# Kernel optimization log

Measured on AMD Instinct MI355X. Metric: run time of the kernel, lower is better.

Reference implementation:

```python
import jax, jax.numpy as jnp
import numpy as np

B, S, H = 2, 2048, 1024
NH, HD = 16, 64  # num_heads, head_size


def setup_inputs() -> dict:
    key = jax.random.key(0)
    ks = jax.random.split(key, 8)
    return {
        "x": jax.random.normal(ks[0], (B, S, H), dtype=jnp.float32),
        "attn_mask": jax.random.randint(ks[1], (B, S, S), 0, 2, dtype=jnp.int32),
        "Wq": jax.random.normal(ks[2], (H, H), dtype=jnp.float32) * 0.02,
        "bq": jax.random.normal(ks[3], (H,), dtype=jnp.float32) * 0.02,
        "Wk": jax.random.normal(ks[4], (H, H), dtype=jnp.float32) * 0.02,
        "bk": jax.random.normal(ks[5], (H,), dtype=jnp.float32) * 0.02,
        "Wv": jax.random.normal(ks[6], (H, H), dtype=jnp.float32) * 0.02,
        "bv": jax.random.normal(ks[7], (H,), dtype=jnp.float32) * 0.02,
    }


def reference(x, attn_mask, Wq, bq, Wk, bk, Wv, bv):
    b, s, h = x.shape
    # QKV projections (self-attention: kv = attention_input)
    q = (jnp.einsum('bih,hx->bix', x, Wq) + bq).reshape(b, s, NH, HD)
    k = (jnp.einsum('bih,hx->bix', x, Wk) + bk).reshape(b, s, NH, HD)
    v = (jnp.einsum('bih,hx->bix', x, Wv) + bv).reshape(b, s, NH, HD)
    scale = 1.0 / (HD ** 0.5)
    # [B, NH, Sq, Skv] score matrix, additive mask, softmax
    attn_score = jnp.einsum('bind,bjnd->bnij', q, k) * scale
    adder = attn_mask.astype(jnp.float32)[:, None, :, :] * -10000.0
    attn_prob = jax.nn.softmax(attn_score + adder, axis=-1)
    # dropout is identity (training=False)
    attn_vec = jnp.einsum('bnij,bjnd->bind', attn_prob, v)
    return attn_vec.reshape(b, s, NH * HD)
```

## Files before the change

### kernel.cpp

```cpp
#include <hip/hip_runtime.h>
#include <hip/hip_bf16.h>
#include <math.h>


#define DI __device__ __forceinline__

typedef unsigned short u16;
typedef unsigned int u32;
typedef unsigned long long u64;
typedef __attribute__((ext_vector_type(8))) short bf16x8;
typedef __attribute__((ext_vector_type(4))) float f32x4;

constexpr int BB = 2, SS = 2048, HH = 1024, NHEAD = 16, HDIM = 64;

DI u16 f2bf(float f) {
  __hip_bfloat16 h = __float2bfloat16(f);
  union { __hip_bfloat16 h; u16 u; } c; c.h = h; return c.u;
}

DI void gload_lds16(const void* g, const void* l) {
  __builtin_amdgcn_global_load_lds(
      (const __attribute__((address_space(1))) u32*)(u64)g,
      (__attribute__((address_space(3))) u32*)(u32)(u64)l,
      16, 0, 0);
}

__global__ void xcast(const float* __restrict__ x, u16* __restrict__ xb) {
  const size_t i = ((size_t)blockIdx.x * 256 + threadIdx.x) * 8;
  float4 f0 = *(const float4*)(x + i);
  float4 f1 = *(const float4*)(x + i + 4);
  bf16x8 v;
  v[0] = (short)f2bf(f0.x); v[1] = (short)f2bf(f0.y);
  v[2] = (short)f2bf(f0.z); v[3] = (short)f2bf(f0.w);
  v[4] = (short)f2bf(f1.x); v[5] = (short)f2bf(f1.y);
  v[6] = (short)f2bf(f1.z); v[7] = (short)f2bf(f1.w);
  *(bf16x8*)(xb + i) = v;
}

__global__ void wtrans(const float* __restrict__ Wq, const float* __restrict__ Wk,
                       const float* __restrict__ Wv, u16* __restrict__ WT) {
  __shared__ u16 tile[64][65];
  const float* W = (blockIdx.z == 0) ? Wq : (blockIdx.z == 1) ? Wk : Wv;
  u16* Wt = WT + (size_t)blockIdx.z * HH * HH;
  const int n0 = blockIdx.x * 64, k0 = blockIdx.y * 64;
  for (int i = threadIdx.x; i < 64 * 64; i += 256) {
    int r = i >> 6, c = i & 63;
    tile[r][c] = f2bf(W[(size_t)(k0 + r) * HH + n0 + c]);
  }
  __syncthreads();
  for (int i = threadIdx.x; i < 64 * 64; i += 256) {
    int r = i >> 6, c = i & 63;
    Wt[(size_t)(n0 + r) * HH + k0 + c] = tile[c][r];
  }
}

__global__ void maskpack(const int* __restrict__ mask, u64* __restrict__ mb) {
  const size_t idx = (size_t)blockIdx.x * 256 + threadIdx.x;
  const int v = mask[idx];
  const u64 bal = __ballot(v != 0);
  if ((threadIdx.x & 63) == 0) mb[idx >> 6] = bal;
}

__global__ __launch_bounds__(256) void qkv_gemm(
    const u16* __restrict__ X, const u16* __restrict__ WTall,
    const float* __restrict__ bq, const float* __restrict__ bk,
    const float* __restrict__ bv,
    u16* __restrict__ Qo, u16* __restrict__ Ko, u16* __restrict__ Vo) {
  __shared__ alignas(128) u16 As[128 * 64];
  __shared__ alignas(128) u16 Bs[128 * 64];

  const int z = blockIdx.z;
  const u16* Wt = WTall + (size_t)z * HH * HH;
  const float* bias = (z == 0) ? bq : (z == 1) ? bk : bv;
  u16* Out = (z == 0) ? Qo : (z == 1) ? Ko : Vo;
  const float oscale = (z == 0) ? 0.18033688011112042f : 1.0f;

  const int tid = threadIdx.x;
  const int lane = tid & 63;
  const int w = tid >> 6;
  const int wm = (w >> 1) * 64, wn = (w & 1) * 64;
  const int lr = lane & 15, lkg = lane >> 4;
  const int m0 = blockIdx.y * 128, n0 = blockIdx.x * 128;

  u32 srow[4], scol[4];
#pragma unroll
  for (int i = 0; i < 4; ++i) {
    u32 f = i * 4096 + w * 1024 + lane * 16;
    u32 g = f ^ (((f >> 7) & 7) << 4);
    srow[i] = g >> 7;
    scol[i] = (g & 127) >> 1;
  }

  u32 aoff[4][2], boff[4][2];
#pragma unroll
  for (int mf = 0; mf < 4; ++mf)
#pragma unroll
    for (int ks = 0; ks < 2; ++ks) {
      int row = wm + mf * 16 + lr;
      aoff[mf][ks] = (u32)((row * 128 + ks * 64 + lkg * 16) ^ ((row & 7) << 4));
      row = wn + mf * 16 + lr;
      boff[mf][ks] = (u32)((row * 128 + ks * 64 + lkg * 16) ^ ((row & 7) << 4));
    }

  f32x4 acc[4][4];
#pragma unroll
  for (int i = 0; i < 4; ++i)
#pragma unroll
    for (int j = 0; j < 4; ++j) acc[i][j] = {0.f, 0.f, 0.f, 0.f};

  const u16* Xb = X + (size_t)m0 * HH;
  const u16* Wb = Wt + (size_t)n0 * HH;

  auto stage = [&](int kt) {
    const int k0 = kt * 64;
#pragma unroll
    for (int i = 0; i < 4; ++i) {
      gload_lds16(Xb + (size_t)srow[i] * HH + k0 + scol[i],
                  (const char*)As + i * 4096 + w * 1024);
      gload_lds16(Wb + (size_t)srow[i] * HH + k0 + scol[i],
                  (const char*)Bs + i * 4096 + w * 1024);
    }
  };

  stage(0);
  const int NT = HH / 64;
  for (int kt = 0; kt < NT; ++kt) {
    __syncthreads();
    bf16x8 a[2][4], bfr[2][4];
#pragma unroll
    for (int ks = 0; ks < 2; ++ks)
#pragma unroll
      for (int i = 0; i < 4; ++i) {
        a[ks][i] = *(const bf16x8*)((const char*)As + aoff[i][ks]);
        bfr[ks][i] = *(const bf16x8*)((const char*)Bs + boff[i][ks]);
      }
    __syncthreads();
    if (kt + 1 < NT) stage(kt + 1);
    __builtin_amdgcn_s_setprio(1);
#pragma unroll
    for (int ks = 0; ks < 2; ++ks)
#pragma unroll
      for (int mf = 0; mf < 4; ++mf)
#pragma unroll
        for (int nf = 0; nf < 4; ++nf)
          acc[mf][nf] = __builtin_amdgcn_mfma_f32_16x16x32_bf16(
              a[ks][mf], bfr[ks][nf], acc[mf][nf], 0, 0, 0);
    __builtin_amdgcn_s_setprio(0);
  }

#pragma unroll
  for (int mf = 0; mf < 4; ++mf)
#pragma unroll
    for (int nf = 0; nf < 4; ++nf) {
      const int gn = n0 + wn + nf * 16 + lr;
      const float bvv = bias[gn];
      const int nh = gn >> 6, hd = gn & 63;
#pragma unroll
      for (int r = 0; r < 4; ++r) {
        const int gm = m0 + wm + mf * 16 + lkg * 4 + r;
        const int bb = gm >> 11, ss = gm & 2047;
        const float v = (acc[mf][nf][r] + bvv) * oscale;
        if (z < 2)
          Out[(((size_t)bb * NHEAD + nh) * SS + ss) * HDIM + hd] = f2bf(v);
        else
          Out[(((size_t)bb * NHEAD + nh) * HDIM + hd) * SS + ss] = f2bf(v);
      }
    }
}

__global__ __launch_bounds__(512) void attn(
    const u16* __restrict__ Q, const u16* __restrict__ K,
    const u16* __restrict__ Vt, const u64* __restrict__ mb,
    float* __restrict__ out) {
  __shared__ alignas(128) char smem[16384 + 16384 + 8 * 16 * 72 * 2];
  u16* Ks = (u16*)smem;
  u16* Vs = (u16*)(smem + 16384);
  typedef u16 PsRow[16][72];
  PsRow* Ps = (PsRow*)(smem + 32768);
  float* cmb = (float*)smem;

  const int nh = blockIdx.x, qt = blockIdx.y, b = blockIdx.z;
  const int bnh = b * NHEAD + nh;
  const u16* Qh = Q + (size_t)bnh * SS * HDIM;
  const u16* Kh = K + (size_t)bnh * SS * HDIM;
  const u16* Vh = Vt + (size_t)bnh * HDIM * SS;
  const int q0 = qt * 64;

  const int tid = threadIdx.x, lane = tid & 63, w = tid >> 6;
  const int g = w >> 2, wg = w & 3;
  const int lr = lane & 15, lkg = lane >> 4;
  const int qrow_lane = q0 + wg * 16 + lr;
  const int kvbase = g * (SS / 2);

  bf16x8 qf[2];
#pragma unroll
  for (int h = 0; h < 2; ++h)
    qf[h] = *(const bf16x8*)(Qh + (size_t)qrow_lane * HDIM + h * 32 + lkg * 8);

  u32 srow[2], scol[2];
#pragma unroll
  for (int i = 0; i < 2; ++i) {
    u32 f = i * 4096 + wg * 1024 + lane * 16;
    u32 gg = f ^ (((f >> 7) & 7) << 4);
    srow[i] = gg >> 7;
    scol[i] = (gg & 127) >> 1;
  }

  auto stage = [&](int t) {
    const int kv0 = kvbase + t * 64;
#pragma unroll
    for (int i = 0; i < 2; ++i) {
      gload_lds16(Kh + (size_t)(kv0 + srow[i]) * HDIM + scol[i],
                  (const char*)(Ks + g * 4096) + i * 4096 + wg * 1024);
      gload_lds16(Vh + (size_t)srow[i] * SS + kv0 + scol[i],
                  (const char*)(Vs + g * 4096) + i * 4096 + wg * 1024);
    }
  };

  u32 koff[4][2];
#pragma unroll
  for (int i = 0; i < 4; ++i)
#pragma unroll
    for (int h = 0; h < 2; ++h) {
      int row = i * 16 + lr;
      koff[i][h] = (u32)((row * 128 + h * 64 + lkg * 16) ^ ((row & 7) << 4));
    }

  bf16x8 ones;
#pragma unroll
  for (int j = 0; j < 8; ++j) ones[j] = (short)0x3F80;

  f32x4 oacc[4];
  f32x4 lacc = {0.f, 0.f, 0.f, 0.f};
#pragma unroll
  for (int n = 0; n < 4; ++n) oacc[n] = {0.f, 0.f, 0.f, 0.f};

  stage(0);
  const int NT = SS / 128;
  const char* Kbase = (const char*)(Ks + g * 4096);
  const char* Vbase = (const char*)(Vs + g * 4096);
  for (int t = 0; t < NT; ++t) {
    __syncthreads();

    const u64 sh =
        mb[((size_t)b * SS + qrow_lane) * (SS / 64) + g * NT + t] >> (lkg * 4);
    const u32 w01 = (u32)sh, w23 = (u32)(sh >> 32);

    f32x4 sacc[4];
#pragma unroll
    for (int kvb = 0; kvb < 4; ++kvb) sacc[kvb] = {0.f, 0.f, 0.f, 0.f};
    __builtin_amdgcn_s_setprio(1);
#pragma unroll
    for (int kvb = 0; kvb < 4; ++kvb)
#pragma unroll
      for (int h = 0; h < 2; ++h) {
        const bf16x8 kf = *(const bf16x8*)(Kbase + koff[kvb][h]);
        sacc[kvb] = __builtin_amdgcn_mfma_f32_16x16x32_bf16(
            kf, qf[h], sacc[kvb], 0, 0, 0);
      }
    __builtin_amdgcn_s_setprio(0);

#pragma unroll
    for (int kvb = 0; kvb < 4; ++kvb) {
      const u32 word = (kvb < 2) ? w01 : w23;
      const int sb = (kvb & 1) * 16;
      union { u16 h[4]; u64 d; } pk;
#pragma unroll
      for (int r = 0; r < 4; ++r) {
        float s = sacc[kvb][r];
        s = ((word >> (sb + r)) & 1u) ? -14000.0f : s;
        pk.h[r] = f2bf(__builtin_amdgcn_exp2f(s));
      }
      *(u64*)&Ps[w][lr][kvb * 16 + lkg * 4] = pk.d;
    }

    __builtin_amdgcn_s_setprio(1);
#pragma unroll
    for (int ks = 0; ks < 2; ++ks) {
      const bf16x8 pf = *(const bf16x8*)&Ps[w][lr][ks * 32 + lkg * 8];
#pragma unroll
      for (int n = 0; n < 4; ++n) {
        const bf16x8 vf = *(const bf16x8*)(Vbase + koff[n][ks]);
        oacc[n] = __builtin_amdgcn_mfma_f32_16x16x32_bf16(
            pf, vf, oacc[n], 0, 0, 0);
      }
      lacc = __builtin_amdgcn_mfma_f32_16x16x32_bf16(pf, ones, lacc, 0, 0, 0);
    }
    __builtin_amdgcn_s_setprio(0);

    __syncthreads();
    if (t + 1 < NT) stage(t + 1);
  }

  const int lid = wg * 64 + lane;
  if (g == 1) {
#pragma unroll
    for (int n = 0; n < 4; ++n)
#pragma unroll
      for (int r = 0; r < 4; ++r) cmb[(n * 4 + r) * 256 + lid] = oacc[n][r];
#pragma unroll
    for (int r = 0; r < 4; ++r) cmb[(16 + r) * 256 + lid] = lacc[r];
  }
  __syncthreads();
  if (g == 0) {
#pragma unroll
    for (int r = 0; r < 4; ++r) {
      const float l = lacc[r] + cmb[(16 + r) * 256 + lid];
      const float rcp = 1.0f / l;
      const int qrow = q0 + wg * 16 + lkg * 4 + r;
#pragma unroll
      for (int n = 0; n < 4; ++n) {
        const float o = oacc[n][r] + cmb[(n * 4 + r) * 256 + lid];
        out[((size_t)b * SS + qrow) * HH + nh * HDIM + n * 16 + lr] = o * rcp;
      }
    }
  }
}

extern "C" void kernel_launch(void* const* d_in, const int* in_sizes, int n_in,
                              void* d_out, int out_size, void* d_ws,
                              size_t ws_size, hipStream_t stream) {
  const float* x = (const float*)d_in[0];
  const int* mask = (const int*)d_in[1];
  const float* Wq = (const float*)d_in[2];
  const float* bq = (const float*)d_in[3];
  const float* Wk = (const float*)d_in[4];
  const float* bk = (const float*)d_in[5];
  const float* Wv = (const float*)d_in[6];
  const float* bv = (const float*)d_in[7];
  float* out = (float*)d_out;

  char* ws = (char*)d_ws;
  const size_t MB = 1024 * 1024;
  u16* Qw = (u16*)(ws + 0 * MB);
  u16* Kw = (u16*)(ws + 8 * MB);
  u16* Vtw = (u16*)(ws + 16 * MB);
  u64* mbp = (u64*)(ws + 24 * MB);
  u16* Xb = (u16*)d_out;
  u16* WT = (u16*)((char*)d_out + 8 * MB);

  xcast<<<dim3((BB * SS * HH) / (256 * 8)), 256, 0, stream>>>(x, Xb);
  wtrans<<<dim3(16, 16, 3), 256, 0, stream>>>(Wq, Wk, Wv, WT);
  maskpack<<<dim3((BB * SS * SS) / 256), 256, 0, stream>>>(mask, mbp);
  qkv_gemm<<<dim3(8, 32, 3), 256, 0, stream>>>(Xb, WT, bq, bk, bv, Qw, Kw, Vtw);
  attn<<<dim3(NHEAD, SS / 64, BB), 512, 0, stream>>>(Qw, Kw, Vtw, mbp, out);
}
```

Measured before the change: 132.0 us.

## Process two 16-row query subtiles per wave to double K/V reuse

Each wave now computes two 16-row query blocks against each staged K/V tile, so every block covers 128 query rows and the grid along the sequence dimension is halved. This halves the global-to-LDS K/V traffic and LDS fragment reads per unit of work. In exchange it uses more accumulator registers and LDS for the P buffer, and launches fewer blocks, which may reduce occupancy.

```diff
diff --git a/kernel.cpp b/kernel.cpp
--- a/kernel.cpp
+++ b/kernel.cpp
@@ -172,10 +172,10 @@
     const u16* __restrict__ Q, const u16* __restrict__ K,
     const u16* __restrict__ Vt, const u64* __restrict__ mb,
     float* __restrict__ out) {
-  __shared__ alignas(128) char smem[16384 + 16384 + 8 * 16 * 72 * 2];
+  __shared__ alignas(128) char smem[16384 + 16384 + 8 * 32 * 72 * 2];
   u16* Ks = (u16*)smem;
   u16* Vs = (u16*)(smem + 16384);
-  typedef u16 PsRow[16][72];
+  typedef u16 PsRow[32][72];
   PsRow* Ps = (PsRow*)(smem + 32768);
   float* cmb = (float*)smem;
 
@@ -184,18 +184,20 @@
   const u16* Qh = Q + (size_t)bnh * SS * HDIM;
   const u16* Kh = K + (size_t)bnh * SS * HDIM;
   const u16* Vh = Vt + (size_t)bnh * HDIM * SS;
-  const int q0 = qt * 64;
+  const int q0 = qt * 128;
 
   const int tid = threadIdx.x, lane = tid & 63, w = tid >> 6;
   const int g = w >> 2, wg = w & 3;
   const int lr = lane & 15, lkg = lane >> 4;
-  const int qrow_lane = q0 + wg * 16 + lr;
   const int kvbase = g * (SS / 2);
 
-  bf16x8 qf[2];
-#pragma unroll
-  for (int h = 0; h < 2; ++h)
-    qf[h] = *(const bf16x8*)(Qh + (size_t)qrow_lane * HDIM + h * 32 + lkg * 8);
+  bf16x8 qf[2][2];
+#pragma unroll
+  for (int m = 0; m < 2; ++m)
+#pragma unroll
+    for (int h = 0; h < 2; ++h)
+      qf[m][h] = *(const bf16x8*)(Qh +
+          (size_t)(q0 + wg * 32 + m * 16 + lr) * HDIM + h * 32 + lkg * 8);
 
   u32 srow[2], scol[2];
 #pragma unroll
@@ -230,10 +232,14 @@
 #pragma unroll
   for (int j = 0; j < 8; ++j) ones[j] = (short)0x3F80;
 
-  f32x4 oacc[4];
-  f32x4 lacc = {0.f, 0.f, 0.f, 0.f};
-#pragma unroll
-  for (int n = 0; n < 4; ++n) oacc[n] = {0.f, 0.f, 0.f, 0.f};
+  f32x4 oacc[2][4];
+  f32x4 lacc[2];
+#pragma unroll
+  for (int m = 0; m < 2; ++m) {
+#pragma unroll
+    for (int n = 0; n < 4; ++n) oacc[m][n] = {0.f, 0.f, 0.f, 0.f};
+    lacc[m] = {0.f, 0.f, 0.f, 0.f};
+  }
 
   stage(0);
   const int NT = SS / 128;
@@ -242,49 +248,68 @@
   for (int t = 0; t < NT; ++t) {
     __syncthreads();
 
-    const u64 sh =
-        mb[((size_t)b * SS + qrow_lane) * (SS / 64) + g * NT + t] >> (lkg * 4);
-    const u32 w01 = (u32)sh, w23 = (u32)(sh >> 32);
-
-    f32x4 sacc[4];
-#pragma unroll
-    for (int kvb = 0; kvb < 4; ++kvb) sacc[kvb] = {0.f, 0.f, 0.f, 0.f};
+    u32 mw[2][2];
+#pragma unroll
+    for (int m = 0; m < 2; ++m) {
+      const u64 sh = mb[((size_t)b * SS + (q0 + wg * 32 + m * 16 + lr)) *
+                        (SS / 64) + g * NT + t] >> (lkg * 4);
+      mw[m][0] = (u32)sh;
+      mw[m][1] = (u32)(sh >> 32);
+    }
+
+    f32x4 sacc[2][4];
+#pragma unroll
+    for (int m = 0; m < 2; ++m)
+#pragma unroll
+      for (int kvb = 0; kvb < 4; ++kvb) sacc[m][kvb] = {0.f, 0.f, 0.f, 0.f};
     __builtin_amdgcn_s_setprio(1);
 #pragma unroll
     for (int kvb = 0; kvb < 4; ++kvb)
 #pragma unroll
       for (int h = 0; h < 2; ++h) {
         const bf16x8 kf = *(const bf16x8*)(Kbase + koff[kvb][h]);
-        sacc[kvb] = __builtin_amdgcn_mfma_f32_16x16x32_bf16(
-            kf, qf[h], sacc[kvb], 0, 0, 0);
+#pragma unroll
+        for (int m = 0; m < 2; ++m)
+          sacc[m][kvb] = __builtin_amdgcn_mfma_f32_16x16x32_bf16(
+              kf, qf[m][h], sacc[m][kvb], 0, 0, 0);
       }
     __builtin_amdgcn_s_setprio(0);
 
 #pragma unroll
-    for (int kvb = 0; kvb < 4; ++kvb) {
-      const u32 word = (kvb < 2) ? w01 : w23;
-      const int sb = (kvb & 1) * 16;
-      union { u16 h[4]; u64 d; } pk;
-#pragma unroll
-      for (int r = 0; r < 4; ++r) {
-        float s = sacc[kvb][r];
-        s = ((word >> (sb + r)) & 1u) ? -14000.0f : s;
-        pk.h[r] = f2bf(__builtin_amdgcn_exp2f(s));
-      }
-      *(u64*)&Ps[w][lr][kvb * 16 + lkg * 4] = pk.d;
-    }
+    for (int m = 0; m < 2; ++m)
+#pragma unroll
+      for (int kvb = 0; kvb < 4; ++kvb) {
+        const u32 word = mw[m][kvb >> 1];
+        const int sb = (kvb & 1) * 16;
+        union { u16 h[4]; u64 d; } pk;
+#pragma unroll
+        for (int r = 0; r < 4; ++r) {
+          float s = sacc[m][kvb][r];
+          s = ((word >> (sb + r)) & 1u) ? -14000.0f : s;
+          pk.h[r] = f2bf(__builtin_amdgcn_exp2f(s));
+        }
+        *(u64*)&Ps[w][m * 16 + lr][kvb * 16 + lkg * 4] = pk.d;
+      }
 
     __builtin_amdgcn_s_setprio(1);
 #pragma unroll
     for (int ks = 0; ks < 2; ++ks) {
-      const bf16x8 pf = *(const bf16x8*)&Ps[w][lr][ks * 32 + lkg * 8];
+      bf16x8 pf[2];
+#pragma unroll
+      for (int m = 0; m < 2; ++m)
+        pf[m] = *(const bf16x8*)&Ps[w][m * 16 + lr][ks * 32 + lkg * 8];
 #pragma unroll
       for (int n = 0; n < 4; ++n) {
         const bf16x8 vf = *(const bf16x8*)(Vbase + koff[n][ks]);
-        oacc[n] = __builtin_amdgcn_mfma_f32_16x16x32_bf16(
-            pf, vf, oacc[n], 0, 0, 0);
-      }
-      lacc = __builtin_amdgcn_mfma_f32_16x16x32_bf16(pf, ones, lacc, 0, 0, 0);
+#pragma unroll
+        for (int m = 0; m < 2; ++m)
+          oacc[m][n] = __builtin_amdgcn_mfma_f32_16x16x32_bf16(
+              pf[m], vf, oacc[m][n], 0, 0, 0);
+      }
+#pragma unroll
+      for (int m = 0; m < 2; ++m)
+        lacc[m] = __builtin_amdgcn_mfma_f32_16x16x32_bf16(
+            pf[m], ones, lacc[m], 0, 0, 0);
     }
     __builtin_amdgcn_s_setprio(0);
 
@@ -295,25 +320,34 @@
   const int lid = wg * 64 + lane;
   if (g == 1) {
 #pragma unroll
-    for (int n = 0; n < 4; ++n)
-#pragma unroll
-      for (int r = 0; r < 4; ++r) cmb[(n * 4 + r) * 256 + lid] = oacc[n][r];
-#pragma unroll
-    for (int r = 0; r < 4; ++r) cmb[(16 + r) * 256 + lid] = lacc[r];
+    for (int m = 0; m < 2; ++m) {
+#pragma unroll
+      for (int n = 0; n < 4; ++n)
+#pragma unroll
+        for (int r = 0; r < 4; ++r)
+          cmb[(m * 16 + n * 4 + r) * 256 + lid] = oacc[m][n][r];
+#pragma unroll
+      for (int r = 0; r < 4; ++r)
+        cmb[(32 + m * 4 + r) * 256 + lid] = lacc[m][r];
+    }
   }
   __syncthreads();
   if (g == 0) {
 #pragma unroll
-    for (int r = 0; r < 4; ++r) {
-      const float l = lacc[r] + cmb[(16 + r) * 256 + lid];
-      const float rcp = 1.0f / l;
-      const int qrow = q0 + wg * 16 + lkg * 4 + r;
-#pragma unroll
-      for (int n = 0; n < 4; ++n) {
-        const float o = oacc[n][r] + cmb[(n * 4 + r) * 256 + lid];
-        out[((size_t)b * SS + qrow) * HH + nh * HDIM + n * 16 + lr] = o * rcp;
-      }
-    }
+    for (int m = 0; m < 2; ++m)
+#pragma unroll
+      for (int r = 0; r < 4; ++r) {
+        const float l = lacc[m][r] + cmb[(32 + m * 4 + r) * 256 + lid];
+        const float rcp = 1.0f / l;
+        const int qrow = q0 + wg * 32 + m * 16 + lkg * 4 + r;
+#pragma unroll
+        for (int n = 0; n < 4; ++n) {
+          const float o =
+              oacc[m][n][r] + cmb[(m * 16 + n * 4 + r) * 256 + lid];
+          out[((size_t)b * SS + qrow) * HH + nh * HDIM + n * 16 + lr] =
+              o * rcp;
+        }
+      }
   }
 }
 
@@ -343,5 +377,5 @@
   wtrans<<<dim3(16, 16, 3), 256, 0, stream>>>(Wq, Wk, Wv, WT);
   maskpack<<<dim3((BB * SS * SS) / 256), 256, 0, stream>>>(mask, mbp);
   qkv_gemm<<<dim3(8, 32, 3), 256, 0, stream>>>(Xb, WT, bq, bk, bv, Qw, Kw, Vtw);
-  attn<<<dim3(NHEAD, SS / 64, BB), 512, 0, stream>>>(Qw, Kw, Vtw, mbp, out);
-}
+  attn<<<dim3(NHEAD, SS / 128, BB), 512, 0, stream>>>(Qw, Kw, Vtw, mbp, out);
+}
```

Result: slower. 146.2 us (+10.8%).
